# Performance work log

Measured on AMD Instinct MI355X. Metric: run time of the kernel, lower is better.

## Reference

```python
import jax, jax.numpy as jnp
import numpy as np

N_NODES = 100000
N_EDGES = 3200000
F_IN, F_HID, F_OUT = 128, 64, 2


def setup_inputs() -> dict:
    key = jax.random.key(0)
    k1, k2, k3, k4 = jax.random.split(key, 4)
    x = jax.random.normal(k1, (N_NODES, F_IN), dtype=jnp.float32)
    edge_index = jax.random.randint(k2, (2, N_EDGES), 0, N_NODES, dtype=jnp.int64)
    W1 = jax.random.normal(k3, (F_IN, F_HID), dtype=jnp.float32) * (1.0 / np.sqrt(F_IN))
    b1 = jnp.zeros((F_HID,), dtype=jnp.float32)
    W2 = jax.random.normal(k4, (F_HID, F_OUT), dtype=jnp.float32) * (1.0 / np.sqrt(F_HID))
    b2 = jnp.zeros((F_OUT,), dtype=jnp.float32)
    return {"x": x, "edge_index": edge_index, "W1": W1, "b1": b1, "W2": W2, "b2": b2}


def _gcn_conv(h, W, b, src, dst, norm, n_nodes):
    # linear transform first (PyG GCNConv does x @ W then propagate)
    h = h @ W                                  # [N, F_out]
    msg = h[src] * norm[:, None]               # gather + per-edge scale, [E+N, F_out]
    agg = jax.ops.segment_sum(msg, dst, num_segments=n_nodes)  # scatter-add
    return agg + b


def reference(x, edge_index, W1, b1, W2, b2):
    n = x.shape[0]
    # add self-loops (GCNConv default add_self_loops=True)
    loops = jnp.arange(n, dtype=edge_index.dtype)
    src = jnp.concatenate([edge_index[0], loops])
    dst = jnp.concatenate([edge_index[1], loops])
    # symmetric degree normalization: deg computed on dst after self-loops
    deg = jax.ops.segment_sum(jnp.ones_like(dst, dtype=x.dtype), dst, num_segments=n)
    dinv = jnp.where(deg > 0, jax.lax.rsqrt(deg), 0.0)
    norm = dinv[src] * dinv[dst]               # [E+N]

    h = _gcn_conv(x, W1, b1, src, dst, norm, n)
    h = jax.nn.relu(h)
    # dropout is identity in eval mode (training=False)
    out = _gcn_conv(h, W2, b2, src, dst, norm, n)  # [N, 2]

    # generator_mask = x[:, 0] == 1; keep static shape by masking + flattening
    mask = (x[:, 0] == 1.0).astype(out.dtype)
    return (out * mask[:, None]).reshape(-1)
```

## Files before the change

### kernel.cpp

```cpp
#include <hip/hip_runtime.h>
#include <hip/hip_bf16.h>
#include <math.h>


constexpr int N   = 100000;
constexpr int E   = 3200000;
constexpr int FIN = 128;
constexpr int FH  = 64;

constexpr int NPB = 256;
constexpr int NB  = (N + NPB - 1) / NPB;
constexpr int K   = 6400;
constexpr int NC  = E / K;
constexpr int NXCD = 8;

typedef __attribute__((ext_vector_type(8))) short short8;
typedef __attribute__((ext_vector_type(4))) float f32x4;
typedef __attribute__((ext_vector_type(2))) float f32x2;

__device__ inline short f2bf(float f) {
  unsigned u = __float_as_uint(f);
  return (short)((u + 0x7FFFu + ((u >> 16) & 1u)) >> 16);
}

__device__ inline unsigned char f2fp8(float f) {
  return (unsigned char)(__builtin_amdgcn_cvt_pk_fp8_f32(f, f, 0, false) & 0xFF);
}

__device__ inline int chunk_of(int bid) {
  const int q = NC / NXCD, r = NC % NXCD;
  int xcd = bid & 7, idx = bid >> 3;
  return (xcd < r) ? xcd * (q + 1) + idx : r * (q + 1) + (xcd - r) * q + idx;
}

__global__ __launch_bounds__(512) void k_cnt(const int* __restrict__ dstA,
                                             int* __restrict__ segCnt) {
  __shared__ int bc[NB];
  const int w = chunk_of(blockIdx.x);
  const int base = w * K;
  for (int i = threadIdx.x; i < NB; i += 512) bc[i] = 0;
  __syncthreads();
  for (int i = threadIdx.x; i < K; i += 512)
    atomicAdd(&bc[dstA[base + i] >> 8], 1);
  __syncthreads();
  for (int b = threadIdx.x; b < NB; b += 512) segCnt[b * NC + w] = bc[b];
}

__global__ __launch_bounds__(512) void k_chunkScan(const int* __restrict__ segCnt,
                                                   int* __restrict__ lp,
                                                   int* __restrict__ binTot) {
  __shared__ int sh[512];
  const int b = blockIdx.x;
  const int t = threadIdx.x;
  int v = (t < NC) ? segCnt[b * NC + t] : 0;
  sh[t] = v;
  __syncthreads();
  for (int off = 1; off < 512; off <<= 1) {
    int tv = (t >= off) ? sh[t - off] : 0;
    __syncthreads();
    sh[t] += tv;
    __syncthreads();
  }
  if (t < NC) lp[b * NC + t] = sh[t] - v;
  if (t == 511) binTot[b] = sh[511];
}

__global__ void k_binScan(const int* __restrict__ binTot,
                          int* __restrict__ binBase, int* __restrict__ rowptr) {
  if (threadIdx.x == 0 && blockIdx.x == 0) {
    int s = 0;
    for (int b = 0; b < NB; ++b) { binBase[b] = s; s += binTot[b]; }
    binBase[NB] = s;
    rowptr[N] = s;
  }
}

__global__ __launch_bounds__(512) void k_scat(const int* __restrict__ srcA,
                                              const int* __restrict__ dstA,
                                              const int* __restrict__ lp,
                                              const int* __restrict__ binBase,
                                              unsigned* __restrict__ binned) {
  __shared__ int lpw[NB];
  __shared__ int cur[NB];
  const int w = chunk_of(blockIdx.x);
  const int base = w * K;
  for (int b = threadIdx.x; b < NB; b += 512) {
    lpw[b] = binBase[b] + lp[b * NC + w];
    cur[b] = 0;
  }
  __syncthreads();
  for (int i = threadIdx.x; i < K; i += 512) {
    int s = srcA[base + i];
    int d = dstA[base + i];
    int b = d >> 8;
    int slot = lpw[b] + atomicAdd(&cur[b], 1);
    binned[slot] = ((unsigned)(d & 255) << 17) | (unsigned)s;
  }
}

__global__ __launch_bounds__(512) void k_fill4(const unsigned* __restrict__ binned,
                                               const int* __restrict__ binBase,
                                               int* __restrict__ rowptr,
                                               float* __restrict__ dinv,
                                               int* __restrict__ csr_src) {
  __shared__ int cnt_s[NPB];
  __shared__ int sh[NPB];
  __shared__ int cur[NPB];
  const int b = blockIdx.x;
  const int t = threadIdx.x;
  const int w0 = binBase[b], w1 = binBase[b + 1];
  if (t < NPB) cnt_s[t] = 0;
  __syncthreads();
  unsigned e0_,e1_,e2_,e3_,e4_,e5_,e6_,e7_,e8_,e9_,e10_,e11_,e12_,e13_,e14_,e15_,e16_;
  unsigned* ebuf[17] = {&e0_,&e1_,&e2_,&e3_,&e4_,&e5_,&e6_,&e7_,&e8_,&e9_,
                        &e10_,&e11_,&e12_,&e13_,&e14_,&e15_,&e16_};
#pragma unroll
  for (int r = 0; r < 17; ++r) {
    int i = w0 + t + r * 512;
    unsigned e = (i < w1) ? binned[i] : 0xFFFFFFFFu;
    *ebuf[r] = e;
    if (e != 0xFFFFFFFFu) atomicAdd(&cnt_s[e >> 17], 1);
  }
  for (int i = w0 + t + 17 * 512; i < w1; i += 512)
    atomicAdd(&cnt_s[binned[i] >> 17], 1);
  __syncthreads();
  int v = 0;
  if (t < NPB) { v = cnt_s[t]; sh[t] = v; }
  __syncthreads();
  for (int off = 1; off < NPB; off <<= 1) {
    int tv = (t < NPB && t >= off) ? sh[t - off] : 0;
    __syncthreads();
    if (t < NPB) sh[t] += tv;
    __syncthreads();
  }
  if (t < NPB) {
    int node = b * NPB + t;
    int start = w0 + sh[t] - v;
    if (node < N) {
      rowptr[node] = start;
      dinv[node] = 1.0f / sqrtf((float)(v + 1));
    }
    cur[t] = start;
  }
  __syncthreads();
#pragma unroll
  for (int r = 0; r < 17; ++r) {
    unsigned e = *ebuf[r];
    if (e != 0xFFFFFFFFu) {
      int p = atomicAdd(&cur[e >> 17], 1);
      csr_src[p] = (int)(e & 0x1FFFFu);
    }
  }
  for (int i = w0 + t + 17 * 512; i < w1; i += 512) {
    unsigned e = binned[i];
    int p = atomicAdd(&cur[e >> 17], 1);
    csr_src[p] = (int)(e & 0x1FFFFu);
  }
}

__global__ __launch_bounds__(256) void k_gemm1(const float* __restrict__ x,
                                               const float* __restrict__ W1,
                                               const float* __restrict__ dinv,
                                               unsigned char* __restrict__ m1) {
  __shared__ short8 W1f[16 * 64];
  const int t = threadIdx.x;
  for (int i = t; i < 16 * 64; i += 256) {
    int frag = i >> 6, l = i & 63;
    int s = frag >> 2, j = frag & 3;
    int kb = 32 * s + 8 * (l >> 4);
    int f  = 16 * j + (l & 15);
    short8 v;
#pragma unroll
    for (int e = 0; e < 8; ++e) v[e] = f2bf(W1[(kb + e) * FH + f]);
    W1f[i] = v;
  }
  __syncthreads();
  const int lane = t & 63;
  const int r16 = lane & 15;
  const int g4  = lane >> 4;
  const int nWaves = gridDim.x * 4;
  const int wid = blockIdx.x * 4 + (t >> 6);
  for (int T = wid; T < N / 16; T += nWaves) {
    const float* xrow = x + (size_t)(16 * T + r16) * FIN + 8 * g4;
    f32x4 acc0 = {0,0,0,0}, acc1 = {0,0,0,0}, acc2 = {0,0,0,0}, acc3 = {0,0,0,0};
#pragma unroll
    for (int s = 0; s < 4; ++s) {
      float4 fa = *(const float4*)(xrow + 32 * s);
      float4 fb = *(const float4*)(xrow + 32 * s + 4);
      short8 a;
      a[0] = f2bf(fa.x); a[1] = f2bf(fa.y); a[2] = f2bf(fa.z); a[3] = f2bf(fa.w);
      a[4] = f2bf(fb.x); a[5] = f2bf(fb.y); a[6] = f2bf(fb.z); a[7] = f2bf(fb.w);
      acc0 = __builtin_amdgcn_mfma_f32_16x16x32_bf16(a, W1f[(s*4+0)*64 + lane], acc0, 0, 0, 0);
      acc1 = __builtin_amdgcn_mfma_f32_16x16x32_bf16(a, W1f[(s*4+1)*64 + lane], acc1, 0, 0, 0);
      acc2 = __builtin_amdgcn_mfma_f32_16x16x32_bf16(a, W1f[(s*4+2)*64 + lane], acc2, 0, 0, 0);
      acc3 = __builtin_amdgcn_mfma_f32_16x16x32_bf16(a, W1f[(s*4+3)*64 + lane], acc3, 0, 0, 0);
    }
    const int nodeBase = 16 * T + 4 * g4;
    float dv0 = dinv[nodeBase + 0];
    float dv1 = dinv[nodeBase + 1];
    float dv2 = dinv[nodeBase + 2];
    float dv3 = dinv[nodeBase + 3];
#pragma unroll
    for (int j = 0; j < 4; ++j) {
      f32x4 acc = (j == 0) ? acc0 : (j == 1) ? acc1 : (j == 2) ? acc2 : acc3;
      size_t fcol = 16 * j + r16;
      m1[(size_t)(nodeBase + 0) * FH + fcol] = f2fp8(acc[0] * dv0);
      m1[(size_t)(nodeBase + 1) * FH + fcol] = f2fp8(acc[1] * dv1);
      m1[(size_t)(nodeBase + 2) * FH + fcol] = f2fp8(acc[2] * dv2);
      m1[(size_t)(nodeBase + 3) * FH + fcol] = f2fp8(acc[3] * dv3);
    }
  }
}

__global__ __launch_bounds__(256) void k_agg1(const unsigned char* __restrict__ m1,
                                              const int* __restrict__ rowptr,
                                              const int* __restrict__ csr_src,
                                              const float* __restrict__ dinv,
                                              const float* __restrict__ b1,
                                              const float* __restrict__ W2,
                                              float* __restrict__ m2) {
  const int lane = threadIdx.x & 63;
  const int half = lane >> 5;
  const int nb   = blockIdx.x * 16 + (threadIdx.x >> 6) * 4;
  const int node0 = nb + half;
  const int node1 = nb + 2 + half;
  const int g2 = (lane >> 3) & 3;
  const int q  = lane & 7;
  const int i  = lane & 31;
  const int s00 = rowptr[node0];
  const int deg0 = rowptr[node0 + 1] - s00;
  const int s01 = rowptr[node1];
  const int deg1 = rowptr[node1 + 1] - s01;
  const uint2* __restrict__ m1q = (const uint2*)m1;
  float x0=0,x1=0,x2=0,x3=0,x4=0,x5=0,x6=0,x7=0;
  float y0=0,y1=0,y2=0,y3=0,y4=0,y5=0,y6=0,y7=0;
  for (int base = 0;; base += 32) {
    int rem0 = deg0 - base, rem1 = deg1 - base;
    if (__all((rem0 <= 0) && (rem1 <= 0))) break;
    int sv0 = (i < rem0) ? csr_src[s00 + base + i] : 0;
    int sv1 = (i < rem1) ? csr_src[s01 + base + i] : 0;
#pragma unroll
    for (int j = 0; j < 32; j += 8) {
      int idx = j + g2;
      int sa = __shfl(sv0, (half << 5) | idx);
      int sb = __shfl(sv1, (half << 5) | idx);
      bool pa = idx < rem0, pb = idx < rem1;
      uint2 va, vb;
      if (pa) va = m1q[(size_t)sa * 8 + q];
      if (pb) vb = m1q[(size_t)sb * 8 + q];
      if (pa) {
        f32x2 f0 = __builtin_amdgcn_cvt_pk_f32_fp8(va.x, false);
        f32x2 f1 = __builtin_amdgcn_cvt_pk_f32_fp8(va.x, true);
        f32x2 f2 = __builtin_amdgcn_cvt_pk_f32_fp8(va.y, false);
        f32x2 f3 = __builtin_amdgcn_cvt_pk_f32_fp8(va.y, true);
        x0 += f0.x; x1 += f0.y; x2 += f1.x; x3 += f1.y;
        x4 += f2.x; x5 += f2.y; x6 += f3.x; x7 += f3.y;
      }
      if (pb) {
        f32x2 f0 = __builtin_amdgcn_cvt_pk_f32_fp8(vb.x, false);
        f32x2 f1 = __builtin_amdgcn_cvt_pk_f32_fp8(vb.x, true);
        f32x2 f2 = __builtin_amdgcn_cvt_pk_f32_fp8(vb.y, false);
        f32x2 f3 = __builtin_amdgcn_cvt_pk_f32_fp8(vb.y, true);
        y0 += f0.x; y1 += f0.y; y2 += f1.x; y3 += f1.y;
        y4 += f2.x; y5 += f2.y; y6 += f3.x; y7 += f3.y;
      }
    }
  }
#pragma unroll
  for (int off = 8; off <= 16; off <<= 1) {
    x0 += __shfl_xor(x0, off); x1 += __shfl_xor(x1, off);
    x2 += __shfl_xor(x2, off); x3 += __shfl_xor(x3, off);
    x4 += __shfl_xor(x4, off); x5 += __shfl_xor(x5, off);
    x6 += __shfl_xor(x6, off); x7 += __shfl_xor(x7, off);
    y0 += __shfl_xor(y0, off); y1 += __shfl_xor(y1, off);
    y2 += __shfl_xor(y2, off); y3 += __shfl_xor(y3, off);
    y4 += __shfl_xor(y4, off); y5 += __shfl_xor(y5, off);
    y6 += __shfl_xor(y6, off); y7 += __shfl_xor(y7, off);
  }
  {
    uint2 va = m1q[(size_t)node0 * 8 + q];
    uint2 vb = m1q[(size_t)node1 * 8 + q];
    f32x2 f0 = __builtin_amdgcn_cvt_pk_f32_fp8(va.x, false);
    f32x2 f1 = __builtin_amdgcn_cvt_pk_f32_fp8(va.x, true);
    f32x2 f2 = __builtin_amdgcn_cvt_pk_f32_fp8(va.y, false);
    f32x2 f3 = __builtin_amdgcn_cvt_pk_f32_fp8(va.y, true);
    x0 += f0.x; x1 += f0.y; x2 += f1.x; x3 += f1.y;
    x4 += f2.x; x5 += f2.y; x6 += f3.x; x7 += f3.y;
    f0 = __builtin_amdgcn_cvt_pk_f32_fp8(vb.x, false);
    f1 = __builtin_amdgcn_cvt_pk_f32_fp8(vb.x, true);
    f2 = __builtin_amdgcn_cvt_pk_f32_fp8(vb.y, false);
    f3 = __builtin_amdgcn_cvt_pk_f32_fp8(vb.y, true);
    y0 += f0.x; y1 += f0.y; y2 += f1.x; y3 += f1.y;
    y4 += f2.x; y5 += f2.y; y6 += f3.x; y7 += f3.y;
  }
  const float4 bva = ((const float4*)b1)[q * 2 + 0];
  const float4 bvb = ((const float4*)b1)[q * 2 + 1];
  const float4 wA = ((const float4*)W2)[q * 4 + 0];
  const float4 wB = ((const float4*)W2)[q * 4 + 1];
  const float4 wC = ((const float4*)W2)[q * 4 + 2];
  const float4 wD = ((const float4*)W2)[q * 4 + 3];
  const float dv0 = dinv[node0];
  const float dv1 = dinv[node1];
  float h0 = fmaxf(fmaf(x0, dv0, bva.x), 0.f);
  float h1 = fmaxf(fmaf(x1, dv0, bva.y), 0.f);
  float h2 = fmaxf(fmaf(x2, dv0, bva.z), 0.f);
  float h3 = fmaxf(fmaf(x3, dv0, bva.w), 0.f);
  float h4 = fmaxf(fmaf(x4, dv0, bvb.x), 0.f);
  float h5 = fmaxf(fmaf(x5, dv0, bvb.y), 0.f);
  float h6 = fmaxf(fmaf(x6, dv0, bvb.z), 0.f);
  float h7 = fmaxf(fmaf(x7, dv0, bvb.w), 0.f);
  float p00 = h0 * wA.x + h1 * wA.z + h2 * wB.x + h3 * wB.z
            + h4 * wC.x + h5 * wC.z + h6 * wD.x + h7 * wD.z;
  float p01 = h0 * wA.y + h1 * wA.w + h2 * wB.y + h3 * wB.w
            + h4 * wC.y + h5 * wC.w + h6 * wD.y + h7 * wD.w;
  h0 = fmaxf(fmaf(y0, dv1, bva.x), 0.f);
  h1 = fmaxf(fmaf(y1, dv1, bva.y), 0.f);
  h2 = fmaxf(fmaf(y2, dv1, bva.z), 0.f);
  h3 = fmaxf(fmaf(y3, dv1, bva.w), 0.f);
  h4 = fmaxf(fmaf(y4, dv1, bvb.x), 0.f);
  h5 = fmaxf(fmaf(y5, dv1, bvb.y), 0.f);
  h6 = fmaxf(fmaf(y6, dv1, bvb.z), 0.f);
  h7 = fmaxf(fmaf(y7, dv1, bvb.w), 0.f);
  float p10 = h0 * wA.x + h1 * wA.z + h2 * wB.x + h3 * wB.z
            + h4 * wC.x + h5 * wC.z + h6 * wD.x + h7 * wD.z;
  float p11 = h0 * wA.y + h1 * wA.w + h2 * wB.y + h3 * wB.w
            + h4 * wC.y + h5 * wC.w + h6 * wD.y + h7 * wD.w;
#pragma unroll
  for (int off = 4; off; off >>= 1) {
    p00 += __shfl_xor(p00, off); p01 += __shfl_xor(p01, off);
    p10 += __shfl_xor(p10, off); p11 += __shfl_xor(p11, off);
  }
  if ((lane & 31) == 0) {
    m2[node0 * 2 + 0] = p00 * dv0;
    m2[node0 * 2 + 1] = p01 * dv0;
    m2[node1 * 2 + 0] = p10 * dv1;
    m2[node1 * 2 + 1] = p11 * dv1;
  }
}

__global__ __launch_bounds__(256) void k_agg2(const float* __restrict__ m2,
                                              const int* __restrict__ rowptr,
                                              const int* __restrict__ csr_src,
                                              const float* __restrict__ dinv,
                                              const float* __restrict__ b2,
                                              const float* __restrict__ x,
                                              float* __restrict__ out) {
  const int lane = threadIdx.x & 63;
  const int half = lane >> 5;
  const int node = blockIdx.x * 8 + (threadIdx.x >> 6) * 2 + half;
  const int s0 = rowptr[node];
  const int e0 = rowptr[node + 1];
  float a0 = 0.f, a1 = 0.f;
  for (int e = s0 + (lane & 31); e < e0; e += 32) {
    int s = csr_src[e];
    a0 += m2[s * 2 + 0];
    a1 += m2[s * 2 + 1];
  }
#pragma unroll
  for (int off = 16; off; off >>= 1) {
    a0 += __shfl_xor(a0, off);
    a1 += __shfl_xor(a1, off);
  }
  if ((lane & 31) == 0) {
    a0 += m2[node * 2 + 0];
    a1 += m2[node * 2 + 1];
    float dv = dinv[node];
    float o0 = a0 * dv + b2[0];
    float o1 = a1 * dv + b2[1];
    float msk = (x[(size_t)node * FIN] == 1.0f) ? 1.0f : 0.0f;
    out[node * 2 + 0] = o0 * msk;
    out[node * 2 + 1] = o1 * msk;
  }
}

extern "C" void kernel_launch(void* const* d_in, const int* in_sizes, int n_in,
                              void* d_out, int out_size, void* d_ws, size_t ws_size,
                              hipStream_t stream) {
  const float* x   = (const float*)d_in[0];
  const int*   ei  = (const int*)d_in[1];
  const float* W1  = (const float*)d_in[2];
  const float* b1  = (const float*)d_in[3];
  const float* W2  = (const float*)d_in[4];
  const float* b2  = (const float*)d_in[5];
  float*       out = (float*)d_out;

  char* w = (char*)d_ws;
  auto alloc = [&](size_t bytes) -> char* {
    char* p = w;
    w += (bytes + 255) & ~(size_t)255;
    return p;
  };
  int*            rowptr  = (int*)alloc((size_t)(N + 1) * 4);
  float*          dinv    = (float*)alloc((size_t)N * 4);
  unsigned*       binned  = (unsigned*)alloc((size_t)E * 4);
  int*            segCnt  = (int*)alloc((size_t)NB * NC * 4);
  int*            lp      = (int*)alloc((size_t)NB * NC * 4);
  int*            binTot  = (int*)alloc((size_t)NB * 4);
  int*            binBase = (int*)alloc((size_t)(NB + 1) * 4);
  int*            csr_src = (int*)alloc((size_t)E * 4);
  unsigned char*  m1      = (unsigned char*)alloc((size_t)N * FH);
  float*          m2      = (float*)alloc((size_t)N * 2 * 4);

  const int* srcA = ei;
  const int* dstA = ei + E;

  k_cnt<<<dim3(NC), dim3(512), 0, stream>>>(dstA, segCnt);
  k_chunkScan<<<dim3(NB), dim3(512), 0, stream>>>(segCnt, lp, binTot);
  k_binScan<<<dim3(1), dim3(64), 0, stream>>>(binTot, binBase, rowptr);
  k_scat<<<dim3(NC), dim3(512), 0, stream>>>(srcA, dstA, lp, binBase, binned);
  k_fill4<<<dim3(NB), dim3(512), 0, stream>>>(binned, binBase, rowptr, dinv, csr_src);
  k_gemm1<<<dim3(800), dim3(256), 0, stream>>>(x, W1, dinv, m1);
  k_agg1<<<dim3(N / 16), dim3(256), 0, stream>>>(m1, rowptr, csr_src, dinv, b1, W2, m2);
  k_agg2<<<dim3(N / 8), dim3(256), 0, stream>>>(m2, rowptr, csr_src, dinv, b2, x, out);
}
```

Measured before the change: 128.9 us.

## Halve edge chunk size, widen chunk scan, vectorize aggregation accumulators

The edge chunk size used by the binning pass is halved, so the count and scatter kernels get twice as many blocks, and the chunk scan is widened to 1024 threads to cover them. Separately, the layer-1 aggregation accumulators become packed float2 vectors so the compiler can emit packed adds. The layer-2 aggregation now loads m2 as float2. The extra blocks improve occupancy but double the segCnt and lp arrays and lengthen the scan.

```diff
diff --git a/kernel.cpp b/kernel.cpp
--- a/kernel.cpp
+++ b/kernel.cpp
@@ -10,7 +10,7 @@
 
 constexpr int NPB = 256;
 constexpr int NB  = (N + NPB - 1) / NPB;
-constexpr int K   = 6400;
+constexpr int K   = 3200;
 constexpr int NC  = E / K;
 constexpr int NXCD = 8;
 
@@ -46,23 +46,23 @@
   for (int b = threadIdx.x; b < NB; b += 512) segCnt[b * NC + w] = bc[b];
 }
 
-__global__ __launch_bounds__(512) void k_chunkScan(const int* __restrict__ segCnt,
-                                                   int* __restrict__ lp,
-                                                   int* __restrict__ binTot) {
-  __shared__ int sh[512];
+__global__ __launch_bounds__(1024) void k_chunkScan(const int* __restrict__ segCnt,
+                                                    int* __restrict__ lp,
+                                                    int* __restrict__ binTot) {
+  __shared__ int sh[1024];
   const int b = blockIdx.x;
   const int t = threadIdx.x;
   int v = (t < NC) ? segCnt[b * NC + t] : 0;
   sh[t] = v;
   __syncthreads();
-  for (int off = 1; off < 512; off <<= 1) {
+  for (int off = 1; off < 1024; off <<= 1) {
     int tv = (t >= off) ? sh[t - off] : 0;
     __syncthreads();
     sh[t] += tv;
     __syncthreads();
   }
   if (t < NC) lp[b * NC + t] = sh[t] - v;
-  if (t == 511) binTot[b] = sh[511];
+  if (t == 1023) binTot[b] = sh[1023];
 }
 
 __global__ void k_binScan(const int* __restrict__ binTot,
@@ -232,8 +232,8 @@
   const int s01 = rowptr[node1];
   const int deg1 = rowptr[node1 + 1] - s01;
   const uint2* __restrict__ m1q = (const uint2*)m1;
-  float x0=0,x1=0,x2=0,x3=0,x4=0,x5=0,x6=0,x7=0;
-  float y0=0,y1=0,y2=0,y3=0,y4=0,y5=0,y6=0,y7=0;
+  f32x2 xA = {0,0}, xB = {0,0}, xC = {0,0}, xD = {0,0};
+  f32x2 yA = {0,0}, yB = {0,0}, yC = {0,0}, yD = {0,0};
   for (int base = 0;; base += 32) {
     int rem0 = deg0 - base, rem1 = deg1 - base;
     if (__all((rem0 <= 0) && (rem1 <= 0))) break;
@@ -249,49 +249,42 @@
       if (pa) va = m1q[(size_t)sa * 8 + q];
       if (pb) vb = m1q[(size_t)sb * 8 + q];
       if (pa) {
-        f32x2 f0 = __builtin_amdgcn_cvt_pk_f32_fp8(va.x, false);
-        f32x2 f1 = __builtin_amdgcn_cvt_pk_f32_fp8(va.x, true);
-        f32x2 f2 = __builtin_amdgcn_cvt_pk_f32_fp8(va.y, false);
-        f32x2 f3 = __builtin_amdgcn_cvt_pk_f32_fp8(va.y, true);
-        x0 += f0.x; x1 += f0.y; x2 += f1.x; x3 += f1.y;
-        x4 += f2.x; x5 += f2.y; x6 += f3.x; x7 += f3.y;
+        xA += __builtin_amdgcn_cvt_pk_f32_fp8(va.x, false);
+        xB += __builtin_amdgcn_cvt_pk_f32_fp8(va.x, true);
+        xC += __builtin_amdgcn_cvt_pk_f32_fp8(va.y, false);
+        xD += __builtin_amdgcn_cvt_pk_f32_fp8(va.y, true);
       }
       if (pb) {
-        f32x2 f0 = __builtin_amdgcn_cvt_pk_f32_fp8(vb.x, false);
-        f32x2 f1 = __builtin_amdgcn_cvt_pk_f32_fp8(vb.x, true);
-        f32x2 f2 = __builtin_amdgcn_cvt_pk_f32_fp8(vb.y, false);
-        f32x2 f3 = __builtin_amdgcn_cvt_pk_f32_fp8(vb.y, true);
-        y0 += f0.x; y1 += f0.y; y2 += f1.x; y3 += f1.y;
-        y4 += f2.x; y5 += f2.y; y6 += f3.x; y7 += f3.y;
+        yA += __builtin_amdgcn_cvt_pk_f32_fp8(vb.x, false);
+        yB += __builtin_amdgcn_cvt_pk_f32_fp8(vb.x, true);
+        yC += __builtin_amdgcn_cvt_pk_f32_fp8(vb.y, false);
+        yD += __builtin_amdgcn_cvt_pk_f32_fp8(vb.y, true);
       }
     }
   }
 #pragma unroll
   for (int off = 8; off <= 16; off <<= 1) {
-    x0 += __shfl_xor(x0, off); x1 += __shfl_xor(x1, off);
-    x2 += __shfl_xor(x2, off); x3 += __shfl_xor(x3, off);
-    x4 += __shfl_xor(x4, off); x5 += __shfl_xor(x5, off);
-    x6 += __shfl_xor(x6, off); x7 += __shfl_xor(x7, off);
-    y0 += __shfl_xor(y0, off); y1 += __shfl_xor(y1, off);
-    y2 += __shfl_xor(y2, off); y3 += __shfl_xor(y3, off);
-    y4 += __shfl_xor(y4, off); y5 += __shfl_xor(y5, off);
-    y6 += __shfl_xor(y6, off); y7 += __shfl_xor(y7, off);
+    f32x2 t;
+    t.x = __shfl_xor(xA.x, off); t.y = __shfl_xor(xA.y, off); xA += t;
+    t.x = __shfl_xor(xB.x, off); t.y = __shfl_xor(xB.y, off); xB += t;
+    t.x = __shfl_xor(xC.x, off); t.y = __shfl_xor(xC.y, off); xC += t;
+    t.x = __shfl_xor(xD.x, off); t.y = __shfl_xor(xD.y, off); xD += t;
+    t.x = __shfl_xor(yA.x, off); t.y = __shfl_xor(yA.y, off); yA += t;
+    t.x = __shfl_xor(yB.x, off); t.y = __shfl_xor(yB.y, off); yB += t;
+    t.x = __shfl_xor(yC.x, off); t.y = __shfl_xor(yC.y, off); yC += t;
+    t.x = __shfl_xor(yD.x, off); t.y = __shfl_xor(yD.y, off); yD += t;
   }
   {
     uint2 va = m1q[(size_t)node0 * 8 + q];
     uint2 vb = m1q[(size_t)node1 * 8 + q];
-    f32x2 f0 = __builtin_amdgcn_cvt_pk_f32_fp8(va.x, false);
-    f32x2 f1 = __builtin_amdgcn_cvt_pk_f32_fp8(va.x, true);
-    f32x2 f2 = __builtin_amdgcn_cvt_pk_f32_fp8(va.y, false);
-    f32x2 f3 = __builtin_amdgcn_cvt_pk_f32_fp8(va.y, true);
-    x0 += f0.x; x1 += f0.y; x2 += f1.x; x3 += f1.y;
-    x4 += f2.x; x5 += f2.y; x6 += f3.x; x7 += f3.y;
-    f0 = __builtin_amdgcn_cvt_pk_f32_fp8(vb.x, false);
-    f1 = __builtin_amdgcn_cvt_pk_f32_fp8(vb.x, true);
-    f2 = __builtin_amdgcn_cvt_pk_f32_fp8(vb.y, false);
-    f3 = __builtin_amdgcn_cvt_pk_f32_fp8(vb.y, true);
-    y0 += f0.x; y1 += f0.y; y2 += f1.x; y3 += f1.y;
-    y4 += f2.x; y5 += f2.y; y6 += f3.x; y7 += f3.y;
+    xA += __builtin_amdgcn_cvt_pk_f32_fp8(va.x, false);
+    xB += __builtin_amdgcn_cvt_pk_f32_fp8(va.x, true);
+    xC += __builtin_amdgcn_cvt_pk_f32_fp8(va.y, false);
+    xD += __builtin_amdgcn_cvt_pk_f32_fp8(va.y, true);
+    yA += __builtin_amdgcn_cvt_pk_f32_fp8(vb.x, false);
+    yB += __builtin_amdgcn_cvt_pk_f32_fp8(vb.x, true);
+    yC += __builtin_amdgcn_cvt_pk_f32_fp8(vb.y, false);
+    yD += __builtin_amdgcn_cvt_pk_f32_fp8(vb.y, true);
   }
   const float4 bva = ((const float4*)b1)[q * 2 + 0];
   const float4 bvb = ((const float4*)b1)[q * 2 + 1];
@@ -301,26 +294,26 @@
   const float4 wD = ((const float4*)W2)[q * 4 + 3];
   const float dv0 = dinv[node0];
   const float dv1 = dinv[node1];
-  float h0 = fmaxf(fmaf(x0, dv0, bva.x), 0.f);
-  float h1 = fmaxf(fmaf(x1, dv0, bva.y), 0.f);
-  float h2 = fmaxf(fmaf(x2, dv0, bva.z), 0.f);
-  float h3 = fmaxf(fmaf(x3, dv0, bva.w), 0.f);
-  float h4 = fmaxf(fmaf(x4, dv0, bvb.x), 0.f);
-  float h5 = fmaxf(fmaf(x5, dv0, bvb.y), 0.f);
-  float h6 = fmaxf(fmaf(x6, dv0, bvb.z), 0.f);
-  float h7 = fmaxf(fmaf(x7, dv0, bvb.w), 0.f);
+  float h0 = fmaxf(fmaf(xA.x, dv0, bva.x), 0.f);
+  float h1 = fmaxf(fmaf(xA.y, dv0, bva.y), 0.f);
+  float h2 = fmaxf(fmaf(xB.x, dv0, bva.z), 0.f);
+  float h3 = fmaxf(fmaf(xB.y, dv0, bva.w), 0.f);
+  float h4 = fmaxf(fmaf(xC.x, dv0, bvb.x), 0.f);
+  float h5 = fmaxf(fmaf(xC.y, dv0, bvb.y), 0.f);
+  float h6 = fmaxf(fmaf(xD.x, dv0, bvb.z), 0.f);
+  float h7 = fmaxf(fmaf(xD.y, dv0, bvb.w), 0.f);
   float p00 = h0 * wA.x + h1 * wA.z + h2 * wB.x + h3 * wB.z
             + h4 * wC.x + h5 * wC.z + h6 * wD.x + h7 * wD.z;
   float p01 = h0 * wA.y + h1 * wA.w + h2 * wB.y + h3 * wB.w
             + h4 * wC.y + h5 * wC.w + h6 * wD.y + h7 * wD.w;
-  h0 = fmaxf(fmaf(y0, dv1, bva.x), 0.f);
-  h1 = fmaxf(fmaf(y1, dv1, bva.y), 0.f);
-  h2 = fmaxf(fmaf(y2, dv1, bva.z), 0.f);
-  h3 = fmaxf(fmaf(y3, dv1, bva.w), 0.f);
-  h4 = fmaxf(fmaf(y4, dv1, bvb.x), 0.f);
-  h5 = fmaxf(fmaf(y5, dv1, bvb.y), 0.f);
-  h6 = fmaxf(fmaf(y6, dv1, bvb.z), 0.f);
-  h7 = fmaxf(fmaf(y7, dv1, bvb.w), 0.f);
+  h0 = fmaxf(fmaf(yA.x, dv1, bva.x), 0.f);
+  h1 = fmaxf(fmaf(yA.y, dv1, bva.y), 0.f);
+  h2 = fmaxf(fmaf(yB.x, dv1, bva.z), 0.f);
+  h3 = fmaxf(fmaf(yB.y, dv1, bva.w), 0.f);
+  h4 = fmaxf(fmaf(yC.x, dv1, bvb.x), 0.f);
+  h5 = fmaxf(fmaf(yC.y, dv1, bvb.y), 0.f);
+  h6 = fmaxf(fmaf(yD.x, dv1, bvb.z), 0.f);
+  h7 = fmaxf(fmaf(yD.y, dv1, bvb.w), 0.f);
   float p10 = h0 * wA.x + h1 * wA.z + h2 * wB.x + h3 * wB.z
             + h4 * wC.x + h5 * wC.z + h6 * wD.x + h7 * wD.z;
   float p11 = h0 * wA.y + h1 * wA.w + h2 * wB.y + h3 * wB.w
@@ -350,20 +343,22 @@
   const int node = blockIdx.x * 8 + (threadIdx.x >> 6) * 2 + half;
   const int s0 = rowptr[node];
   const int e0 = rowptr[node + 1];
-  float a0 = 0.f, a1 = 0.f;
+  f32x2 a = {0.f, 0.f};
   for (int e = s0 + (lane & 31); e < e0; e += 32) {
     int s = csr_src[e];
-    a0 += m2[s * 2 + 0];
-    a1 += m2[s * 2 + 1];
+    float2 v = ((const float2*)m2)[s];
+    f32x2 vv; vv.x = v.x; vv.y = v.y;
+    a += vv;
   }
 #pragma unroll
   for (int off = 16; off; off >>= 1) {
-    a0 += __shfl_xor(a0, off);
-    a1 += __shfl_xor(a1, off);
+    f32x2 t;
+    t.x = __shfl_xor(a.x, off); t.y = __shfl_xor(a.y, off);
+    a += t;
   }
   if ((lane & 31) == 0) {
-    a0 += m2[node * 2 + 0];
-    a1 += m2[node * 2 + 1];
+    float a0 = a.x + m2[node * 2 + 0];
+    float a1 = a.y + m2[node * 2 + 1];
     float dv = dinv[node];
     float o0 = a0 * dv + b2[0];
     float o1 = a1 * dv + b2[1];
@@ -405,7 +400,7 @@
   const int* dstA = ei + E;
 
   k_cnt<<<dim3(NC), dim3(512), 0, stream>>>(dstA, segCnt);
-  k_chunkScan<<<dim3(NB), dim3(512), 0, stream>>>(segCnt, lp, binTot);
+  k_chunkScan<<<dim3(NB), dim3(1024), 0, stream>>>(segCnt, lp, binTot);
   k_binScan<<<dim3(1), dim3(64), 0, stream>>>(binTot, binBase, rowptr);
   k_scat<<<dim3(NC), dim3(512), 0, stream>>>(srcA, dstA, lp, binBase, binned);
   k_fill4<<<dim3(NB), dim3(512), 0, stream>>>(binned, binBase, rowptr, dinv, csr_src);
```

New measurement: 132.0 us. +2.5%, slower.
